# Performance work log

Measured on AMD Instinct MI355X. Metric: run time of the kernel, lower is better.

## Reference

```python
import jax, jax.numpy as jnp
import numpy as np

N_NODES = 4096
EMB_DIM = 512
N_HEADS = 8
K_SPARSE = 128
HEAD_DIM = EMB_DIM // N_HEADS


def setup_inputs() -> dict:
    key = jax.random.key(0)
    k1, k2, k3, k4 = jax.random.split(key, 4)
    # xavier_uniform bound for square [D, D] weight
    bound = float(np.sqrt(6.0 / (EMB_DIM + EMB_DIM)))
    return {
        "embedding_matrix": jax.random.normal(k1, (N_NODES, EMB_DIM), dtype=jnp.float32),
        "Wq": jax.random.uniform(k2, (EMB_DIM, EMB_DIM), minval=-bound, maxval=bound, dtype=jnp.float32),
        "bq": jnp.zeros((EMB_DIM,), dtype=jnp.float32),
        "Wk": jax.random.uniform(k3, (EMB_DIM, EMB_DIM), minval=-bound, maxval=bound, dtype=jnp.float32),
        "bk": jnp.zeros((EMB_DIM,), dtype=jnp.float32),
        "sparse_indices": jax.random.randint(k4, (N_HEADS, N_NODES, K_SPARSE), 0, N_NODES, dtype=jnp.int32),
    }


def reference(embedding_matrix, Wq, bq, Wk, bk, sparse_indices):
    N, D = embedding_matrix.shape
    H, _, K = sparse_indices.shape
    hd = D // H
    # torch Linear: y = x @ W.T + b
    q = (embedding_matrix @ Wq.T + bq).reshape(N, H, hd).transpose(1, 0, 2)  # [H, N, hd]
    kk = (embedding_matrix @ Wk.T + bk).reshape(N, H, hd).transpose(1, 0, 2)  # [H, N, hd]
    # per-head gather of K random keys per query node: [H, N, K, hd]
    sel = jax.vmap(lambda kh, ih: kh[ih])(kk, sparse_indices)
    scores = jnp.einsum("hnd,hnkd->hnk", q, sel) / jnp.sqrt(jnp.float32(hd))  # [H, N, K]
    h_idx = jnp.arange(H)[:, None, None]
    n_idx = jnp.arange(N)[None, :, None]
    out = jnp.zeros((H, N, N), dtype=scores.dtype).at[h_idx, n_idx, sparse_indices].set(scores)
    return out
```

## Files before the change

kernel.cpp:

```cpp
#include <hip/hip_runtime.h>
#include <hip/hip_bf16.h>
#include <stdint.h>

#define N_NODES  4096
#define EMB_DIM  512
#define N_HEADS  8
#define K_SPARSE 128
#define HEAD_DIM 64

typedef __attribute__((ext_vector_type(8))) __bf16 bf16x8;
typedef __attribute__((ext_vector_type(4))) float  f32x4;

__device__ __forceinline__ float bf2f(unsigned short u) {
    union { unsigned int i; float f; } v;
    v.i = ((unsigned int)u) << 16;
    return v.f;
}

__device__ __forceinline__ unsigned short f2bf(float f) {
    union { float f; unsigned int i; } v;
    v.f = f;
    unsigned int x = v.i;
    unsigned int rounding = 0x7fffu + ((x >> 16) & 1u);
    x += rounding;
    return (unsigned short)(x >> 16);
}

__global__ __launch_bounds__(256) void proj_kernel(
    const float* __restrict__ X,
    const float* __restrict__ Wq, const float* __restrict__ bq,
    const float* __restrict__ Wk, const float* __restrict__ bk,
    unsigned short* __restrict__ Qb, unsigned short* __restrict__ Kb)
{
    __shared__ unsigned short As[128][40];
    __shared__ unsigned short Bs[128][40];

    const float* __restrict__ W    = blockIdx.z ? Wk : Wq;
    const float* __restrict__ bias = blockIdx.z ? bk : bq;
    unsigned short* __restrict__ out = blockIdx.z ? Kb : Qb;

    const int t    = threadIdx.x;
    const int M0   = blockIdx.x * 128;
    const int N0   = blockIdx.y * 128;
    const int lane = t & 63;
    const int wave = t >> 6;
    const int wm   = (wave >> 1) * 64;
    const int wn   = (wave & 1) * 64;

    const int lr = t >> 1;
    const int lc = (t & 1) * 16;

    f32x4 acc[4][4] = {};

    for (int kt = 0; kt < EMB_DIM / 32; ++kt) {
        const int k0 = kt * 32;
        {
            const float4* srcA = (const float4*)(X + (size_t)(M0 + lr) * EMB_DIM + k0 + lc);
            const float4* srcB = (const float4*)(W + (size_t)(N0 + lr) * EMB_DIM + k0 + lc);
            unsigned int pa[8], pb[8];
            #pragma unroll
            for (int c = 0; c < 4; ++c) {
                float4 va = srcA[c];
                float4 vb = srcB[c];
                pa[c * 2 + 0] = (unsigned int)f2bf(va.x) | ((unsigned int)f2bf(va.y) << 16);
                pa[c * 2 + 1] = (unsigned int)f2bf(va.z) | ((unsigned int)f2bf(va.w) << 16);
                pb[c * 2 + 0] = (unsigned int)f2bf(vb.x) | ((unsigned int)f2bf(vb.y) << 16);
                pb[c * 2 + 1] = (unsigned int)f2bf(vb.z) | ((unsigned int)f2bf(vb.w) << 16);
            }
            uint4* dstA = (uint4*)&As[lr][lc];
            uint4* dstB = (uint4*)&Bs[lr][lc];
            dstA[0] = make_uint4(pa[0], pa[1], pa[2], pa[3]);
            dstA[1] = make_uint4(pa[4], pa[5], pa[6], pa[7]);
            dstB[0] = make_uint4(pb[0], pb[1], pb[2], pb[3]);
            dstB[1] = make_uint4(pb[4], pb[5], pb[6], pb[7]);
        }
        __syncthreads();

        bf16x8 af[4], bff[4];
        #pragma unroll
        for (int i = 0; i < 4; ++i) {
            uint4 a = *(const uint4*)&As[wm + i * 16 + (lane & 15)][(lane >> 4) * 8];
            uint4 b = *(const uint4*)&Bs[wn + i * 16 + (lane & 15)][(lane >> 4) * 8];
            af[i]  = __builtin_bit_cast(bf16x8, a);
            bff[i] = __builtin_bit_cast(bf16x8, b);
        }
        #pragma unroll
        for (int mi = 0; mi < 4; ++mi)
            #pragma unroll
            for (int ni = 0; ni < 4; ++ni)
                acc[mi][ni] = __builtin_amdgcn_mfma_f32_16x16x32_bf16(
                    af[mi], bff[ni], acc[mi][ni], 0, 0, 0);
        __syncthreads();
    }

    #pragma unroll
    for (int mi = 0; mi < 4; ++mi) {
        #pragma unroll
        for (int ni = 0; ni < 4; ++ni) {
            const int col = N0 + wn + ni * 16 + (lane & 15);
            const float bval = bias[col];
            #pragma unroll
            for (int r = 0; r < 4; ++r) {
                const int row = M0 + wm + mi * 16 + (lane >> 4) * 4 + r;
                out[(size_t)row * EMB_DIM + col] = f2bf(acc[mi][ni][r] + bval);
            }
        }
    }
}

__global__ __launch_bounds__(256) void scatter_kernel(
    const unsigned short* __restrict__ Qb,
    const unsigned short* __restrict__ Kb,
    const int* __restrict__ sidx,
    float* __restrict__ out)
{
    __shared__ float rowbuf[N_NODES];
    __shared__ int   sIdx[K_SPARSE];
    __shared__ float qv[HEAD_DIM];

    const int t = threadIdx.x;
    const int b = blockIdx.x;
    const int h = b >> 12;
    const int n = b & (N_NODES - 1);

    float4* rowv = (float4*)rowbuf;
    float4 z4; z4.x = z4.y = z4.z = z4.w = 0.0f;
    #pragma unroll
    for (int i = 0; i < 4; ++i) rowv[t + 256 * i] = z4;

    if (t < K_SPARSE)
        sIdx[t] = sidx[((size_t)(h * N_NODES + n)) * K_SPARSE + t];
    if (t < HEAD_DIM)
        qv[t] = bf2f(Qb[(size_t)n * EMB_DIM + h * HEAD_DIM + t]);
    __syncthreads();

    const int k     = t >> 1;
    const int half  = t & 1;
    const int myidx = sIdx[k];

    unsigned int* tags = (unsigned int*)rowbuf;
    if (half == 0) atomicMax(&tags[myidx], (unsigned int)(k + 1));

    const uint4* krow = (const uint4*)(Kb + (size_t)myidx * EMB_DIM + h * HEAD_DIM + half * 32);
    float acc = 0.0f;
    #pragma unroll
    for (int c = 0; c < 4; ++c) {
        uint4 u = krow[c];
        unsigned int uu[4] = {u.x, u.y, u.z, u.w};
        #pragma unroll
        for (int j = 0; j < 4; ++j) {
            float lo = bf2f((unsigned short)(uu[j] & 0xffffu));
            float hi = bf2f((unsigned short)(uu[j] >> 16));
            acc += lo * qv[half * 32 + c * 8 + j * 2 + 0];
            acc += hi * qv[half * 32 + c * 8 + j * 2 + 1];
        }
    }
    acc += __shfl_xor(acc, 1);

    __syncthreads();

    const bool win = (half == 0) && (tags[myidx] == (unsigned int)(k + 1));
    const float score = acc * 0.125f;

    __syncthreads();

    if (win) rowbuf[myidx] = score;

    __syncthreads();

    float4* orowv = (float4*)(out + ((size_t)(h * N_NODES + n)) * N_NODES);
    #pragma unroll
    for (int i = 0; i < 4; ++i) orowv[t + 256 * i] = rowv[t + 256 * i];
}

extern "C" void kernel_launch(void* const* d_in, const int* in_sizes, int n_in,
                              void* d_out, int out_size, void* d_ws, size_t ws_size,
                              hipStream_t stream) {
    const float* emb = (const float*)d_in[0];
    const float* Wq  = (const float*)d_in[1];
    const float* bq  = (const float*)d_in[2];
    const float* Wk  = (const float*)d_in[3];
    const float* bk  = (const float*)d_in[4];
    const int*   si  = (const int*)d_in[5];
    float* out = (float*)d_out;

    unsigned short* Qb = (unsigned short*)d_ws;
    unsigned short* Kb = Qb + (size_t)N_NODES * EMB_DIM;

    dim3 pg(N_NODES / 128, EMB_DIM / 128, 2);
    proj_kernel<<<pg, 256, 0, stream>>>(emb, Wq, bq, Wk, bk, Qb, Kb);

    scatter_kernel<<<N_HEADS * N_NODES, 256, 0, stream>>>(Qb, Kb, si, out);
}
```

Before: 614.7 us.

## Shrink projection M-tile, hoist index loads, use nontemporal output stores

The projection GEMM tile drops from 128 to 64 rows, doubling the grid so more CUs get work on the small GEMM. The scatter kernel issues its index and query global loads before zeroing the shared row buffer, hiding their latency. It also writes the dense 512MB output with nontemporal stores to avoid polluting the cache. The main cost is the huge output write, so the nontemporal store is the main lever. The smaller tile lowers per-block reuse.

Result: faster. 582.0 us (-5.3%).

```diff
diff --git a/kernel.cpp b/kernel.cpp
--- a/kernel.cpp
+++ b/kernel.cpp
@@ -32,7 +32,7 @@
     const float* __restrict__ Wk, const float* __restrict__ bk,
     unsigned short* __restrict__ Qb, unsigned short* __restrict__ Kb)
 {
-    __shared__ unsigned short As[128][40];
+    __shared__ unsigned short As[64][40];
     __shared__ unsigned short Bs[128][40];
 
     const float* __restrict__ W    = blockIdx.z ? Wk : Wq;
@@ -40,52 +40,58 @@
     unsigned short* __restrict__ out = blockIdx.z ? Kb : Qb;
 
     const int t    = threadIdx.x;
-    const int M0   = blockIdx.x * 128;
+    const int M0   = blockIdx.x * 64;
     const int N0   = blockIdx.y * 128;
     const int lane = t & 63;
     const int wave = t >> 6;
-    const int wm   = (wave >> 1) * 64;
+    const int wm   = (wave >> 1) * 32;
     const int wn   = (wave & 1) * 64;
 
-    const int lr = t >> 1;
-    const int lc = (t & 1) * 16;
-
-    f32x4 acc[4][4] = {};
+    const int arow = t >> 2;
+    const int acol = (t & 3) * 8;
+    const int brow = t >> 1;
+    const int bcol = (t & 1) * 16;
+
+    f32x4 acc[2][4] = {};
 
     for (int kt = 0; kt < EMB_DIM / 32; ++kt) {
         const int k0 = kt * 32;
         {
-            const float4* srcA = (const float4*)(X + (size_t)(M0 + lr) * EMB_DIM + k0 + lc);
-            const float4* srcB = (const float4*)(W + (size_t)(N0 + lr) * EMB_DIM + k0 + lc);
-            unsigned int pa[8], pb[8];
+            const float4* srcA = (const float4*)(X + (size_t)(M0 + arow) * EMB_DIM + k0 + acol);
+            float4 va0 = srcA[0], va1 = srcA[1];
+            unsigned int pa[4];
+            pa[0] = (unsigned int)f2bf(va0.x) | ((unsigned int)f2bf(va0.y) << 16);
+            pa[1] = (unsigned int)f2bf(va0.z) | ((unsigned int)f2bf(va0.w) << 16);
+            pa[2] = (unsigned int)f2bf(va1.x) | ((unsigned int)f2bf(va1.y) << 16);
+            pa[3] = (unsigned int)f2bf(va1.z) | ((unsigned int)f2bf(va1.w) << 16);
+            *(uint4*)&As[arow][acol] = make_uint4(pa[0], pa[1], pa[2], pa[3]);
+
+            const float4* srcB = (const float4*)(W + (size_t)(N0 + brow) * EMB_DIM + k0 + bcol);
+            unsigned int pb[8];
             #pragma unroll
             for (int c = 0; c < 4; ++c) {
-                float4 va = srcA[c];
                 float4 vb = srcB[c];
-                pa[c * 2 + 0] = (unsigned int)f2bf(va.x) | ((unsigned int)f2bf(va.y) << 16);
-                pa[c * 2 + 1] = (unsigned int)f2bf(va.z) | ((unsigned int)f2bf(va.w) << 16);
                 pb[c * 2 + 0] = (unsigned int)f2bf(vb.x) | ((unsigned int)f2bf(vb.y) << 16);
                 pb[c * 2 + 1] = (unsigned int)f2bf(vb.z) | ((unsigned int)f2bf(vb.w) << 16);
             }
-            uint4* dstA = (uint4*)&As[lr][lc];
-            uint4* dstB = (uint4*)&Bs[lr][lc];
-            dstA[0] = make_uint4(pa[0], pa[1], pa[2], pa[3]);
-            dstA[1] = make_uint4(pa[4], pa[5], pa[6], pa[7]);
+            uint4* dstB = (uint4*)&Bs[brow][bcol];
             dstB[0] = make_uint4(pb[0], pb[1], pb[2], pb[3]);
             dstB[1] = make_uint4(pb[4], pb[5], pb[6], pb[7]);
         }
         __syncthreads();
 
-        bf16x8 af[4], bff[4];
-        #pragma unroll
-        for (int i = 0; i < 4; ++i) {
-            uint4 a = *(const uint4*)&As[wm + i * 16 + (lane & 15)][(lane >> 4) * 8];
-            uint4 b = *(const uint4*)&Bs[wn + i * 16 + (lane & 15)][(lane >> 4) * 8];
-            af[i]  = __builtin_bit_cast(bf16x8, a);
-            bff[i] = __builtin_bit_cast(bf16x8, b);
-        }
-        #pragma unroll
-        for (int mi = 0; mi < 4; ++mi)
+        bf16x8 af[2], bff[4];
+        #pragma unroll
+        for (int i = 0; i < 2; ++i)
+            af[i] = __builtin_bit_cast(bf16x8,
+                *(const uint4*)&As[wm + i * 16 + (lane & 15)][(lane >> 4) * 8]);
+        #pragma unroll
+        for (int i = 0; i < 4; ++i)
+            bff[i] = __builtin_bit_cast(bf16x8,
+                *(const uint4*)&Bs[wn + i * 16 + (lane & 15)][(lane >> 4) * 8]);
+
+        #pragma unroll
+        for (int mi = 0; mi < 2; ++mi)
             #pragma unroll
             for (int ni = 0; ni < 4; ++ni)
                 acc[mi][ni] = __builtin_amdgcn_mfma_f32_16x16x32_bf16(
@@ -94,7 +100,7 @@
     }
 
     #pragma unroll
-    for (int mi = 0; mi < 4; ++mi) {
+    for (int mi = 0; mi < 2; ++mi) {
         #pragma unroll
         for (int ni = 0; ni < 4; ++ni) {
             const int col = N0 + wn + ni * 16 + (lane & 15);
@@ -123,15 +129,20 @@
     const int h = b >> 12;
     const int n = b & (N_NODES - 1);
 
-    float4* rowv = (float4*)rowbuf;
-    float4 z4; z4.x = z4.y = z4.z = z4.w = 0.0f;
+    int   myIdxLd = 0;
+    float myQLd   = 0.0f;
+    if (t < K_SPARSE)
+        myIdxLd = sidx[((size_t)(h * N_NODES + n)) * K_SPARSE + t];
+    if (t < HEAD_DIM)
+        myQLd = bf2f(Qb[(size_t)n * EMB_DIM + h * HEAD_DIM + t]);
+
+    f32x4* rowv = (f32x4*)rowbuf;
+    const f32x4 z4 = {0.0f, 0.0f, 0.0f, 0.0f};
     #pragma unroll
     for (int i = 0; i < 4; ++i) rowv[t + 256 * i] = z4;
 
-    if (t < K_SPARSE)
-        sIdx[t] = sidx[((size_t)(h * N_NODES + n)) * K_SPARSE + t];
-    if (t < HEAD_DIM)
-        qv[t] = bf2f(Qb[(size_t)n * EMB_DIM + h * HEAD_DIM + t]);
+    if (t < K_SPARSE) sIdx[t] = myIdxLd;
+    if (t < HEAD_DIM) qv[t]   = myQLd;
     __syncthreads();
 
     const int k     = t >> 1;
@@ -168,9 +179,10 @@
 
     __syncthreads();
 
-    float4* orowv = (float4*)(out + ((size_t)(h * N_NODES + n)) * N_NODES);
-    #pragma unroll
-    for (int i = 0; i < 4; ++i) orowv[t + 256 * i] = rowv[t + 256 * i];
+    f32x4* orowv = (f32x4*)(out + ((size_t)(h * N_NODES + n)) * N_NODES);
+    #pragma unroll
+    for (int i = 0; i < 4; ++i)
+        __builtin_nontemporal_store(rowv[t + 256 * i], &orowv[t + 256 * i]);
 }
 
 extern "C" void kernel_launch(void* const* d_in, const int* in_sizes, int n_in,
@@ -187,7 +199,7 @@
     unsigned short* Qb = (unsigned short*)d_ws;
     unsigned short* Kb = Qb + (size_t)N_NODES * EMB_DIM;
 
-    dim3 pg(N_NODES / 128, EMB_DIM / 128, 2);
+    dim3 pg(N_NODES / 64, EMB_DIM / 128, 2);
     proj_kernel<<<pg, 256, 0, stream>>>(emb, Wq, bq, Wk, bk, Qb, Kb);
 
     scatter_kernel<<<N_HEADS * N_NODES, 256, 0, stream>>>(Qb, Kb, si, out);
```
